# Kernel optimization log

Measured on AMD Instinct MI355X. Metric: run time of the kernel, lower is better.

## Reference

```python
import jax, jax.numpy as jnp
import numpy as np

B, D, E, H, L = 32768, 512, 10, 128, 2  # batch, input_dim, max_charts, expert hidden, latent_dim
RH1, RH2 = 256, 128                      # router hidden sizes
TAU = 3.0


def setup_inputs() -> dict:
    key = jax.random.key(0)
    ks = jax.random.split(key, 16)
    rnd = lambda k, *s: (jax.random.normal(k, s, jnp.float32) * 0.05)
    return {
        "x": jax.random.normal(ks[0], (B, D), jnp.float32),
        "u": jax.random.uniform(ks[1], (B, E), jnp.float32),
        # router params (last layer init ~ N(0, 0.01), bias 0, as in _init_router)
        "rw1": rnd(ks[2], D, RH1), "rb1": jnp.zeros((RH1,), jnp.float32),
        "rw2": rnd(ks[3], RH1, RH2), "rb2": jnp.zeros((RH2,), jnp.float32),
        "rw3": jax.random.normal(ks[4], (RH2, E), jnp.float32) * 0.01,
        "rb3": jnp.zeros((E,), jnp.float32),
        # stacked expert params: all 10 experts batched along leading dim
        "ew1": rnd(ks[5], E, D, H), "eb1": rnd(ks[6], E, H),
        "ew2": rnd(ks[7], E, H, H), "eb2": rnd(ks[8], E, H),
        "ew3": rnd(ks[9], E, H, L), "eb3": rnd(ks[10], E, L),
    }


def reference(x, u, rw1, rb1, rw2, rb2, rw3, rb3, ew1, eb1, ew2, eb2, ew3, eb3):
    # router MLP: D -> 256 -> 128 -> E
    h = jax.nn.relu(x @ rw1 + rb1)
    h = jax.nn.relu(h @ rw2 + rb2)
    logits = h @ rw3 + rb3                                  # [B, E]
    # gumbel_softmax(tau=3.0, hard=False): softmax((logits + gumbel)/tau)
    g = -jnp.log(-jnp.log(jnp.clip(u, 1e-10, 1.0)) + 1e-10)
    weights = jax.nn.softmax((logits + g) / TAU, axis=1)    # [B, E]
    # all 10 experts as batched GEMMs (fuses the python loop over charts)
    h1 = jax.nn.relu(jnp.einsum('bi,eio->beo', x, ew1) + eb1[None])   # [B, E, H]
    h2 = jax.nn.relu(jnp.einsum('beh,eho->beo', h1, ew2) + eb2[None]) # [B, E, H]
    zc = jnp.einsum('beh,ehl->bel', h2, ew3) + eb3[None]              # [B, E, L]
    z = jnp.einsum('be,bel->bl', weights, zc)                         # [B, L]
    chart_outputs = jnp.transpose(zc, (1, 0, 2))                      # [E, B, L]
    return z, weights, chart_outputs
```

## Files before the change

kernel.cpp:

```cpp
#include <hip/hip_runtime.h>
#include <stdint.h>

typedef __bf16 bf16x8 __attribute__((ext_vector_type(8)));
typedef float floatx4 __attribute__((ext_vector_type(4)));
typedef unsigned short ushort_t;

__device__ __forceinline__ ushort_t bf16rne(float f) {
    union { float f; unsigned u; } v; v.f = f;
    return (ushort_t)((v.u + 0x7fffu + ((v.u >> 16) & 1u)) >> 16);
}

__device__ __forceinline__ void gl_lds16(const ushort_t* g, ushort_t* l) {
    __builtin_amdgcn_global_load_lds(
        (const __attribute__((address_space(1))) unsigned int*)g,
        (__attribute__((address_space(3))) unsigned int*)l, 16, 0, 0);
}


#define WAIT_VM_LG_BAR(n) do { asm volatile("s_waitcnt vmcnt(" #n ") lgkmcnt(0)" ::: "memory"); __builtin_amdgcn_s_barrier(); } while (0)
#define WAIT_LG_BAR()     do { asm volatile("s_waitcnt lgkmcnt(0)" ::: "memory"); __builtin_amdgcn_s_barrier(); } while (0)

__global__ void prep(const float* __restrict__ x, ushort_t* __restrict__ x16,
                     const float* __restrict__ ew1, ushort_t* __restrict__ ew1t,
                     const float* __restrict__ ew2, ushort_t* __restrict__ ew2t,
                     const float* __restrict__ rw1, ushort_t* __restrict__ rw1t,
                     const float* __restrict__ rw2, ushort_t* __restrict__ rw2t) {
    __shared__ ushort_t sT[64 * 65];
    int b = blockIdx.x, tid = threadIdx.x;
    if (b < 16384) {
        int i = b * 256 + tid;
        float4 f = ((const float4*)x)[i];
        union { ushort_t s[4]; uint2 v; } pk;
        pk.s[0] = bf16rne(f.x); pk.s[1] = bf16rne(f.y);
        pk.s[2] = bf16rne(f.z); pk.s[3] = bf16rne(f.w);
        ((uint2*)x16)[i] = pk.v;
        return;
    }
    const float* in; ushort_t* outp; int K, N, k0, n0;
    int i = b - 16384;
    if (i < 160) {
        int e = i >> 4, t = i & 15;
        in = ew1 + e * 65536; outp = ew1t + e * 65536;
        K = 512; N = 128; k0 = (t >> 1) * 64; n0 = (t & 1) * 64;
    } else if (i < 200) {
        i -= 160; int e = i >> 2, t = i & 3;
        in = ew2 + e * 16384; outp = ew2t + e * 16384;
        K = 128; N = 128; k0 = (t >> 1) * 64; n0 = (t & 1) * 64;
    } else if (i < 232) {
        i -= 200; in = rw1; outp = rw1t;
        K = 512; N = 256; k0 = (i >> 2) * 64; n0 = (i & 3) * 64;
    } else {
        i -= 232; in = rw2; outp = rw2t;
        K = 256; N = 128; k0 = (i >> 1) * 64; n0 = (i & 1) * 64;
    }
    {
        int c = tid & 63, r0 = tid >> 6;
#pragma unroll
        for (int p = 0; p < 16; ++p) {
            int r = r0 * 16 + p;
            sT[c * 65 + r] = bf16rne(in[(size_t)(k0 + r) * N + n0 + c]);
        }
        __syncthreads();
        int rr = tid & 63, c0 = tid >> 6;
#pragma unroll
        for (int p = 0; p < 16; ++p) {
            int cc = c0 * 16 + p;
            outp[(size_t)(n0 + cc) * K + k0 + rr] = sT[cc * 65 + rr];
        }
    }
}

__global__ __launch_bounds__(256, 2)
void fused_main(const ushort_t* __restrict__ x16,
                const ushort_t* __restrict__ rw1t, const float* __restrict__ rb1,
                const ushort_t* __restrict__ rw2t, const float* __restrict__ rb2,
                const float* __restrict__ rw3, const float* __restrict__ rb3,
                const float* __restrict__ u,
                const ushort_t* __restrict__ ew1t, const ushort_t* __restrict__ ew2t,
                const float* __restrict__ eb1, const float* __restrict__ eb2,
                const float* __restrict__ ew3, const float* __restrict__ eb3,
                float* __restrict__ wts, float* __restrict__ chart) {
    __shared__ alignas(16) ushort_t sU[24576];
    __shared__ float sB1[2][128];
    __shared__ float sB2[2][128];
    __shared__ float sW3e[2][256];
    __shared__ float zbuf[128][2];

    const int tid = threadIdx.x;
    const int id = blockIdx.x;
    const int wave = tid >> 6, lane = tid & 63;
    const int ln15 = lane & 15, q = lane >> 4;
    const int wm = (wave & 1) * 64, wn = (wave >> 1) * 64;
    const int mhalf = wm >> 6, nhalf = wn >> 6;
    const int rl = lane >> 2, cl = lane & 3;
    const int sw = (cl ^ ((rl >> 1) & 3)) * 8;
    const int rg0 = wave * 2, rg1 = rg0 + 1;
    const int fslot = (4 * ln15 + (q ^ ((ln15 >> 1) & 3))) * 8;

    if (id < 256) {
        const int rb = (id & 7) * 32 + (id >> 3);
        if (tid < 128) sB2[0][tid] = rb2[tid];
        else sB2[1][tid - 128] = rb2[tid];
        const ushort_t* xblk = x16 + (size_t)rb * 128 * 512;

        auto stage_rt = [&](int dst, int k0, const ushort_t* w1base) {
            gl_lds16(xblk + (size_t)(rg0 * 16 + rl) * 512 + k0 + sw, &sU[dst + rg0 * 512]);
            gl_lds16(xblk + (size_t)(rg1 * 16 + rl) * 512 + k0 + sw, &sU[dst + rg1 * 512]);
            gl_lds16(w1base + (size_t)(rg0 * 16 + rl) * 512 + k0 + sw, &sU[dst + 4096 + rg0 * 512]);
            gl_lds16(w1base + (size_t)(rg1 * 16 + rl) * 512 + k0 + sw, &sU[dst + 4096 + rg1 * 512]);
        };
        auto stage_rw2 = [&](int dst, int kh, int ph) {
#pragma unroll
            for (int r = 0; r < 2; ++r) {
                int s = wave * 2 + r;
                gl_lds16(rw2t + (size_t)(s * 16 + rl) * 256 + ph * 128 + kh * 32 + sw,
                         &sU[dst + s * 512]);
            }
        };

        floatx4 acc2[4][4];
#pragma unroll
        for (int i = 0; i < 4; ++i)
#pragma unroll
            for (int j = 0; j < 4; ++j) acc2[i][j] = (floatx4){0.f, 0.f, 0.f, 0.f};

        auto comp_rg2 = [&](int rbase, int kh) {
            bf16x8 a[4], b[4];
#pragma unroll
            for (int t = 0; t < 4; ++t) a[t] = *(const bf16x8*)(&sU[rbase + (mhalf * 4 + t) * 512 + fslot]);
#pragma unroll
            for (int t = 0; t < 4; ++t) b[t] = *(const bf16x8*)(&sU[8192 + kh * 4096 + (nhalf * 4 + t) * 512 + lane * 8]);
            __builtin_amdgcn_s_setprio(1);
#pragma unroll
            for (int i = 0; i < 4; ++i)
#pragma unroll
                for (int j = 0; j < 4; ++j)
                    acc2[i][j] = __builtin_amdgcn_mfma_f32_16x16x32_bf16(a[i], b[j], acc2[i][j], 0, 0, 0);
            __builtin_amdgcn_s_setprio(0);
        };

        for (int ph = 0; ph < 2; ++ph) {
            const ushort_t* w1base = rw1t + (size_t)ph * 65536;
            if (tid < 128) sB1[0][tid] = rb1[ph * 128 + tid];

            floatx4 acc[4][4];
#pragma unroll
            for (int i = 0; i < 4; ++i)
#pragma unroll
                for (int j = 0; j < 4; ++j) acc[i][j] = (floatx4){0.f, 0.f, 0.f, 0.f};

            auto comp_rt = [&](int base) {
                bf16x8 a[4], b[4];
#pragma unroll
                for (int t = 0; t < 4; ++t) a[t] = *(const bf16x8*)(&sU[base + 4096 + (mhalf * 4 + t) * 512 + fslot]);
#pragma unroll
                for (int t = 0; t < 4; ++t) b[t] = *(const bf16x8*)(&sU[base + (nhalf * 4 + t) * 512 + fslot]);
                __builtin_amdgcn_s_setprio(1);
#pragma unroll
                for (int i = 0; i < 4; ++i)
#pragma unroll
                    for (int j = 0; j < 4; ++j)
                        acc[i][j] = __builtin_amdgcn_mfma_f32_16x16x32_bf16(a[i], b[j], acc[i][j], 0, 0, 0);
                __builtin_amdgcn_s_setprio(0);
            };

            stage_rt(0, 0, w1base);
            WAIT_VM_LG_BAR(0);
#pragma unroll 1
            for (int p = 0; p < 8; ++p) {
                int k0 = p * 64;
                stage_rt(8192, k0 + 32, w1base);
                comp_rt(0);
                WAIT_VM_LG_BAR(0);
                if (p < 7) {
                    stage_rt(0, k0 + 64, w1base);
                    comp_rt(8192);
                    WAIT_VM_LG_BAR(0);
                }
            }
            stage_rw2(0, 0, ph);
            comp_rt(8192);
            WAIT_LG_BAR();

#pragma unroll
            for (int i = 0; i < 4; ++i) {
                int hbase = wm + 16 * i;
                int kh = hbase >> 5;
                int qhi = (hbase >> 4) & 1;
                int slotq = 2 * qhi + (q >> 1);
                int h0 = hbase + q * 4;
#pragma unroll
                for (int j = 0; j < 4; ++j) {
                    union { ushort_t s[4]; uint2 v; } pk;
#pragma unroll
                    for (int r = 0; r < 4; ++r)
                        pk.s[r] = bf16rne(fmaxf(acc[i][j][r] + sB1[0][h0 + r], 0.f));
                    *(uint2*)(&sU[8192 + kh * 4096 + (nhalf * 4 + j) * 512 + slotq * 128 + ln15 * 8 + (q & 1) * 4]) = pk.v;
                }
            }

            WAIT_VM_LG_BAR(0);
            stage_rw2(4096, 1, ph); comp_rg2(0, 0);    WAIT_VM_LG_BAR(0);
            stage_rw2(0, 2, ph);    comp_rg2(4096, 1); WAIT_VM_LG_BAR(0);
            stage_rw2(4096, 3, ph); comp_rg2(0, 2);    WAIT_VM_LG_BAR(0);
            comp_rg2(4096, 3);
            WAIT_LG_BAR();
        }

        float* sw3r = (float*)sU;
        float* lgbuf = (float*)(&sU[2560]);
        for (int i = tid; i < 1280; i += 256) sw3r[i] = rw3[i];
        __syncthreads();

        float lg[4][10];
#pragma unroll
        for (int j = 0; j < 4; ++j)
#pragma unroll
            for (int ee = 0; ee < 10; ++ee) lg[j][ee] = 0.f;
#pragma unroll
        for (int i = 0; i < 4; ++i) {
#pragma unroll
            for (int r = 0; r < 4; ++r) {
                int n = wm + i * 16 + q * 4 + r;
                float bias = n < 128 ? sB2[0][n] : sB2[1][n - 128];
                const float* w3r = &sw3r[n * 10];
#pragma unroll
                for (int j = 0; j < 4; ++j) {
                    float val = fmaxf(acc2[i][j][r] + bias, 0.f);
#pragma unroll
                    for (int ee = 0; ee < 10; ++ee) lg[j][ee] += val * w3r[ee];
                }
            }
        }
#pragma unroll
        for (int j = 0; j < 4; ++j)
#pragma unroll
            for (int ee = 0; ee < 10; ++ee) {
                lg[j][ee] += __shfl_xor(lg[j][ee], 16, 64);
                lg[j][ee] += __shfl_xor(lg[j][ee], 32, 64);
            }
        if (wm == 0 && q == 0) {
#pragma unroll
            for (int j = 0; j < 4; ++j) {
                int row = wn + 16 * j + ln15;
#pragma unroll
                for (int ee = 0; ee < 10; ++ee) lgbuf[row * 10 + ee] = lg[j][ee];
            }
        }
        __syncthreads();
        if (wm == 64 && q == 0) {
#pragma unroll
            for (int j = 0; j < 4; ++j) {
                int row = wn + 16 * j + ln15;
#pragma unroll
                for (int ee = 0; ee < 10; ++ee) lgbuf[row * 10 + ee] += lg[j][ee];
            }
        }
        __syncthreads();
        if (tid < 128) {
            int grow = rb * 128 + tid;
            float v[10], mx = -1e30f;
#pragma unroll
            for (int ee = 0; ee < 10; ++ee) {
                float uu = u[(size_t)grow * 10 + ee];
                uu = fminf(fmaxf(uu, 1e-10f), 1.0f);
                float g = -logf(-logf(uu) + 1e-10f);
                v[ee] = (lgbuf[tid * 10 + ee] + rb3[ee] + g) * (1.0f / 3.0f);
                mx = fmaxf(mx, v[ee]);
            }
            float s = 0.f;
#pragma unroll
            for (int ee = 0; ee < 10; ++ee) { v[ee] = expf(v[ee] - mx); s += v[ee]; }
            float inv = 1.0f / s;
#pragma unroll
            for (int ee = 0; ee < 10; ++ee) wts[(size_t)grow * 10 + ee] = v[ee] * inv;
        }
    } else {
        const int eid = id - 256;
        const int xcd = eid & 7, local = eid >> 3;
        const int pr = local % 5;
        const int rb = xcd * 32 + local / 5;
        const int e0 = pr * 2;

        if (tid < 128) {
            sB1[0][tid] = eb1[e0 * 128 + tid];
            sB2[0][tid] = eb2[e0 * 128 + tid];
        } else {
            sB1[1][tid - 128] = eb1[(e0 + 1) * 128 + (tid - 128)];
            sB2[1][tid - 128] = eb2[(e0 + 1) * 128 + (tid - 128)];
        }
        sW3e[0][tid] = ew3[e0 * 256 + tid];
        sW3e[1][tid] = ew3[(e0 + 1) * 256 + tid];

        const ushort_t* xblk = x16 + (size_t)rb * 128 * 512;
        const ushort_t* w1a = ew1t + (size_t)e0 * 65536;
        const ushort_t* w1b = w1a + 65536;

        floatx4 accA[4][4], accB[4][4];
#pragma unroll
        for (int i = 0; i < 4; ++i)
#pragma unroll
            for (int j = 0; j < 4; ++j) {
                accA[i][j] = (floatx4){0.f, 0.f, 0.f, 0.f};
                accB[i][j] = (floatx4){0.f, 0.f, 0.f, 0.f};
            }

        auto stage_g1 = [&](int dst, int k0) {
            gl_lds16(xblk + (size_t)(rg0 * 16 + rl) * 512 + k0 + sw, &sU[dst + rg0 * 512]);
            gl_lds16(xblk + (size_t)(rg1 * 16 + rl) * 512 + k0 + sw, &sU[dst + rg1 * 512]);
            gl_lds16(w1a + (size_t)(rg0 * 16 + rl) * 512 + k0 + sw, &sU[dst + 4096 + rg0 * 512]);
            gl_lds16(w1a + (size_t)(rg1 * 16 + rl) * 512 + k0 + sw, &sU[dst + 4096 + rg1 * 512]);
            gl_lds16(w1b + (size_t)(rg0 * 16 + rl) * 512 + k0 + sw, &sU[dst + 8192 + rg0 * 512]);
            gl_lds16(w1b + (size_t)(rg1 * 16 + rl) * 512 + k0 + sw, &sU[dst + 8192 + rg1 * 512]);
        };
        auto comp_g1 = [&](int base) {
            bf16x8 a0[4], a1[4], b[4];
#pragma unroll
            for (int t = 0; t < 4; ++t) b[t] = *(const bf16x8*)(&sU[base + (nhalf * 4 + t) * 512 + fslot]);
#pragma unroll
            for (int t = 0; t < 4; ++t) a0[t] = *(const bf16x8*)(&sU[base + 4096 + (mhalf * 4 + t) * 512 + fslot]);
#pragma unroll
            for (int t = 0; t < 4; ++t) a1[t] = *(const bf16x8*)(&sU[base + 8192 + (mhalf * 4 + t) * 512 + fslot]);
            __builtin_amdgcn_s_setprio(1);
#pragma unroll
            for (int i = 0; i < 4; ++i)
#pragma unroll
                for (int j = 0; j < 4; ++j) {
                    accA[i][j] = __builtin_amdgcn_mfma_f32_16x16x32_bf16(a0[i], b[j], accA[i][j], 0, 0, 0);
                    accB[i][j] = __builtin_amdgcn_mfma_f32_16x16x32_bf16(a1[i], b[j], accB[i][j], 0, 0, 0);
                }
            __builtin_amdgcn_s_setprio(0);
        };
        auto stage_w2 = [&](const ushort_t* w2, int dst, int kh) {
#pragma unroll
            for (int r = 0; r < 2; ++r) {
                int s = wave * 2 + r;
                gl_lds16(w2 + (size_t)(s * 16 + rl) * 128 + kh * 32 + sw, &sU[dst + s * 512]);
            }
        };
        auto comp_g2 = [&](int rbase, int kh, floatx4 (&acc2)[4][4]) {
            bf16x8 a[4], b[4];
#pragma unroll
            for (int t = 0; t < 4; ++t) a[t] = *(const bf16x8*)(&sU[rbase + (mhalf * 4 + t) * 512 + fslot]);
#pragma unroll
            for (int t = 0; t < 4; ++t) b[t] = *(const bf16x8*)(&sU[8192 + kh * 4096 + (nhalf * 4 + t) * 512 + lane * 8]);
            __builtin_amdgcn_s_setprio(1);
#pragma unroll
            for (int i = 0; i < 4; ++i)
#pragma unroll
                for (int j = 0; j < 4; ++j)
                    acc2[i][j] = __builtin_amdgcn_mfma_f32_16x16x32_bf16(a[i], b[j], acc2[i][j], 0, 0, 0);
            __builtin_amdgcn_s_setprio(0);
        };

        stage_g1(0, 0);
        WAIT_VM_LG_BAR(0);
#pragma unroll 1
        for (int p = 0; p < 8; ++p) {
            int k0 = p * 64;
            stage_g1(12288, k0 + 32);
            comp_g1(0);
            WAIT_VM_LG_BAR(0);
            if (p < 7) {
                stage_g1(0, k0 + 64);
                comp_g1(12288);
                WAIT_VM_LG_BAR(0);
            }
        }
        stage_w2(ew2t + (size_t)e0 * 16384, 0, 0);
        comp_g1(12288);
        WAIT_LG_BAR();

#pragma unroll
        for (int ex = 0; ex < 2; ++ex) {
            const int e = e0 + ex;
            const ushort_t* w2 = ew2t + (size_t)e * 16384;

#pragma unroll
            for (int i = 0; i < 4; ++i) {
                int hbase = wm + 16 * i;
                int kh = hbase >> 5;
                int qhi = (hbase >> 4) & 1;
                int slotq = 2 * qhi + (q >> 1);
                int h0 = hbase + q * 4;
#pragma unroll
                for (int j = 0; j < 4; ++j) {
                    union { ushort_t s[4]; uint2 v; } pk;
#pragma unroll
                    for (int r = 0; r < 4; ++r) {
                        float av = ex == 0 ? accA[i][j][r] : accB[i][j][r];
                        pk.s[r] = bf16rne(fmaxf(av + sB1[ex][h0 + r], 0.f));
                    }
                    *(uint2*)(&sU[8192 + kh * 4096 + (nhalf * 4 + j) * 512 + slotq * 128 + ln15 * 8 + (q & 1) * 4]) = pk.v;
                }
            }

            floatx4 acc2[4][4];
#pragma unroll
            for (int i = 0; i < 4; ++i)
#pragma unroll
                for (int j = 0; j < 4; ++j) acc2[i][j] = (floatx4){0.f, 0.f, 0.f, 0.f};

            WAIT_VM_LG_BAR(0);
            stage_w2(w2, 4096, 1); comp_g2(0, 0, acc2);    WAIT_VM_LG_BAR(0);
            stage_w2(w2, 0, 2);    comp_g2(4096, 1, acc2); WAIT_VM_LG_BAR(0);
            stage_w2(w2, 4096, 3); comp_g2(0, 2, acc2);    WAIT_VM_LG_BAR(0);
            if (ex == 0) stage_w2(ew2t + (size_t)(e0 + 1) * 16384, 0, 0);
            comp_g2(4096, 3, acc2);

            float zc0[4] = {0.f, 0.f, 0.f, 0.f}, zc1[4] = {0.f, 0.f, 0.f, 0.f};
#pragma unroll
            for (int i = 0; i < 4; ++i) {
                int o0 = wm + i * 16 + q * 4;
#pragma unroll
                for (int r = 0; r < 4; ++r) {
                    int o = o0 + r;
                    float w3a = sW3e[ex][2 * o], w3b = sW3e[ex][2 * o + 1];
                    float bias = sB2[ex][o];
#pragma unroll
                    for (int j = 0; j < 4; ++j) {
                        float val = fmaxf(acc2[i][j][r] + bias, 0.f);
                        zc0[j] += val * w3a;
                        zc1[j] += val * w3b;
                    }
                }
            }
#pragma unroll
            for (int j = 0; j < 4; ++j) {
                zc0[j] += __shfl_xor(zc0[j], 16, 64);
                zc0[j] += __shfl_xor(zc0[j], 32, 64);
                zc1[j] += __shfl_xor(zc1[j], 16, 64);
                zc1[j] += __shfl_xor(zc1[j], 32, 64);
            }
            if (wm == 0 && q == 0) {
#pragma unroll
                for (int j = 0; j < 4; ++j) {
                    int row = wn + j * 16 + ln15;
                    zbuf[row][0] = zc0[j];
                    zbuf[row][1] = zc1[j];
                }
            }
            __syncthreads();
            if (wm == 64 && q == 0) {
#pragma unroll
                for (int j = 0; j < 4; ++j) {
                    int row = wn + j * 16 + ln15;
                    zbuf[row][0] += zc0[j];
                    zbuf[row][1] += zc1[j];
                }
            }
            __syncthreads();
            {
                int row = tid >> 1, l = tid & 1;
                int grow = rb * 128 + row;
                chart[(size_t)e * 65536 + (size_t)grow * 2 + l] = zbuf[row][l] + eb3[e * 2 + l];
            }
        }
    }
}

__global__ void z_final(const float* __restrict__ w, const float* __restrict__ chart,
                        float* __restrict__ z) {
    __shared__ float swt[2560];
    int b0 = blockIdx.x * 256;
    for (int i = threadIdx.x; i < 2560; i += 256) swt[i] = w[(size_t)b0 * 10 + i];
    __syncthreads();
    int row = b0 + threadIdx.x;
    float z0 = 0.f, z1 = 0.f;
#pragma unroll
    for (int e = 0; e < 10; ++e) {
        float we = swt[threadIdx.x * 10 + e];
        float2 c = *(const float2*)(&chart[(size_t)e * 65536 + (size_t)row * 2]);
        z0 += we * c.x;
        z1 += we * c.y;
    }
    float2 o; o.x = z0; o.y = z1;
    *(float2*)(&z[(size_t)row * 2]) = o;
}

extern "C" void kernel_launch(void* const* d_in, const int* in_sizes, int n_in,
                              void* d_out, int out_size, void* d_ws, size_t ws_size,
                              hipStream_t stream) {
    const float* x = (const float*)d_in[0];
    const float* u = (const float*)d_in[1];
    const float* rw1 = (const float*)d_in[2];
    const float* rb1 = (const float*)d_in[3];
    const float* rw2 = (const float*)d_in[4];
    const float* rb2 = (const float*)d_in[5];
    const float* rw3 = (const float*)d_in[6];
    const float* rb3 = (const float*)d_in[7];
    const float* ew1 = (const float*)d_in[8];
    const float* eb1 = (const float*)d_in[9];
    const float* ew2 = (const float*)d_in[10];
    const float* eb2 = (const float*)d_in[11];
    const float* ew3 = (const float*)d_in[12];
    const float* eb3 = (const float*)d_in[13];
    float* out = (float*)d_out;
    float* z = out;
    float* wts = out + 65536;
    float* chart = out + 393216;

    ushort_t* x16  = (ushort_t*)d_ws;
    ushort_t* ew1t = x16 + 16777216;
    ushort_t* ew2t = ew1t + 655360;
    ushort_t* rw1t = ew2t + 163840;
    ushort_t* rw2t = rw1t + 131072;

    prep<<<16624, 256, 0, stream>>>(x, x16, ew1, ew1t, ew2, ew2t, rw1, rw1t, rw2, rw2t);

    fused_main<<<1536, 256, 0, stream>>>(x16, rw1t, rb1, rw2t, rb2, rw3, rb3, u,
                                         ew1t, ew2t, eb1, eb2, ew3, eb3,
                                         wts, chart);

    z_final<<<128, 256, 0, stream>>>(wts, chart, z);
}
```

Baseline: 205.8 us.

## Triple-buffer K-loop staging and halve second-layer stage/barrier count

Grows the shared buffer so the first-layer GEMM loops in both router and expert paths use three LDS stages with partial vmcnt waits, keeping two loads in flight instead of one. The second-layer weight staging now loads two K-chunks per stage, so four stage/barrier rounds become two. Router bias loading is hoisted out of the phase loop. Larger LDS use (about 72KB per block) may limit occupancy at two blocks per CU.

```diff
diff --git a/kernel.cpp b/kernel.cpp
--- a/kernel.cpp
+++ b/kernel.cpp
@@ -80,7 +80,7 @@
                 const float* __restrict__ eb1, const float* __restrict__ eb2,
                 const float* __restrict__ ew3, const float* __restrict__ eb3,
                 float* __restrict__ wts, float* __restrict__ chart) {
-    __shared__ alignas(16) ushort_t sU[24576];
+    __shared__ alignas(16) ushort_t sU[36864];
     __shared__ float sB1[2][128];
     __shared__ float sB2[2][128];
     __shared__ float sW3e[2][256];
@@ -99,6 +99,7 @@
 
     if (id < 256) {
         const int rb = (id & 7) * 32 + (id >> 3);
+        sB1[tid >> 7][tid & 127] = rb1[tid];
         if (tid < 128) sB2[0][tid] = rb2[tid];
         else sB2[1][tid - 128] = rb2[tid];
         const ushort_t* xblk = x16 + (size_t)rb * 128 * 512;
@@ -109,12 +110,14 @@
             gl_lds16(w1base + (size_t)(rg0 * 16 + rl) * 512 + k0 + sw, &sU[dst + 4096 + rg0 * 512]);
             gl_lds16(w1base + (size_t)(rg1 * 16 + rl) * 512 + k0 + sw, &sU[dst + 4096 + rg1 * 512]);
         };
-        auto stage_rw2 = [&](int dst, int kh, int ph) {
-#pragma unroll
-            for (int r = 0; r < 2; ++r) {
-                int s = wave * 2 + r;
-                gl_lds16(rw2t + (size_t)(s * 16 + rl) * 256 + ph * 128 + kh * 32 + sw,
-                         &sU[dst + s * 512]);
+        auto stage_rw2 = [&](int reg, int half, int ph) {
+#pragma unroll
+            for (int r = 0; r < 4; ++r) {
+                int s = wave * 4 + r;
+                int khl = s >> 3, rg = s & 7;
+                int kh = half * 2 + khl;
+                gl_lds16(rw2t + (size_t)(rg * 16 + rl) * 256 + ph * 128 + kh * 32 + sw,
+                         &sU[reg + s * 512]);
             }
         };
 
@@ -124,24 +127,27 @@
 #pragma unroll
             for (int j = 0; j < 4; ++j) acc2[i][j] = (floatx4){0.f, 0.f, 0.f, 0.f};
 
-        auto comp_rg2 = [&](int rbase, int kh) {
-            bf16x8 a[4], b[4];
-#pragma unroll
-            for (int t = 0; t < 4; ++t) a[t] = *(const bf16x8*)(&sU[rbase + (mhalf * 4 + t) * 512 + fslot]);
-#pragma unroll
-            for (int t = 0; t < 4; ++t) b[t] = *(const bf16x8*)(&sU[8192 + kh * 4096 + (nhalf * 4 + t) * 512 + lane * 8]);
-            __builtin_amdgcn_s_setprio(1);
-#pragma unroll
-            for (int i = 0; i < 4; ++i)
-#pragma unroll
-                for (int j = 0; j < 4; ++j)
-                    acc2[i][j] = __builtin_amdgcn_mfma_f32_16x16x32_bf16(a[i], b[j], acc2[i][j], 0, 0, 0);
-            __builtin_amdgcn_s_setprio(0);
+        auto comp_rg2 = [&](int reg, int half) {
+#pragma unroll
+            for (int khl = 0; khl < 2; ++khl) {
+                int kh = half * 2 + khl;
+                bf16x8 a[4], b[4];
+#pragma unroll
+                for (int t = 0; t < 4; ++t) a[t] = *(const bf16x8*)(&sU[reg + (khl * 8 + mhalf * 4 + t) * 512 + fslot]);
+#pragma unroll
+                for (int t = 0; t < 4; ++t) b[t] = *(const bf16x8*)(&sU[8192 + kh * 4096 + (nhalf * 4 + t) * 512 + lane * 8]);
+                __builtin_amdgcn_s_setprio(1);
+#pragma unroll
+                for (int i = 0; i < 4; ++i)
+#pragma unroll
+                    for (int j = 0; j < 4; ++j)
+                        acc2[i][j] = __builtin_amdgcn_mfma_f32_16x16x32_bf16(a[i], b[j], acc2[i][j], 0, 0, 0);
+                __builtin_amdgcn_s_setprio(0);
+            }
         };
 
         for (int ph = 0; ph < 2; ++ph) {
             const ushort_t* w1base = rw1t + (size_t)ph * 65536;
-            if (tid < 128) sB1[0][tid] = rb1[ph * 128 + tid];
 
             floatx4 acc[4][4];
 #pragma unroll
@@ -165,22 +171,19 @@
             };
 
             stage_rt(0, 0, w1base);
-            WAIT_VM_LG_BAR(0);
+            stage_rt(8192, 32, w1base);
+            int cb = 0, sb = 16384;
 #pragma unroll 1
-            for (int p = 0; p < 8; ++p) {
-                int k0 = p * 64;
-                stage_rt(8192, k0 + 32, w1base);
-                comp_rt(0);
-                WAIT_VM_LG_BAR(0);
-                if (p < 7) {
-                    stage_rt(0, k0 + 64, w1base);
-                    comp_rt(8192);
-                    WAIT_VM_LG_BAR(0);
-                }
-            }
+            for (int p = 0; p < 16; ++p) {
+                if (p < 15) { WAIT_VM_LG_BAR(4); } else { WAIT_VM_LG_BAR(0); }
+                if (p < 14) stage_rt(sb, (p + 2) * 32, w1base);
+                comp_rt(cb);
+                cb = cb == 16384 ? 0 : cb + 8192;
+                sb = sb == 16384 ? 0 : sb + 8192;
+            }
+            WAIT_LG_BAR();
+
             stage_rw2(0, 0, ph);
-            comp_rt(8192);
-            WAIT_LG_BAR();
 
 #pragma unroll
             for (int i = 0; i < 4; ++i) {
@@ -194,16 +197,16 @@
                     union { ushort_t s[4]; uint2 v; } pk;
 #pragma unroll
                     for (int r = 0; r < 4; ++r)
-                        pk.s[r] = bf16rne(fmaxf(acc[i][j][r] + sB1[0][h0 + r], 0.f));
+                        pk.s[r] = bf16rne(fmaxf(acc[i][j][r] + sB1[ph][h0 + r], 0.f));
                     *(uint2*)(&sU[8192 + kh * 4096 + (nhalf * 4 + j) * 512 + slotq * 128 + ln15 * 8 + (q & 1) * 4]) = pk.v;
                 }
             }
 
             WAIT_VM_LG_BAR(0);
-            stage_rw2(4096, 1, ph); comp_rg2(0, 0);    WAIT_VM_LG_BAR(0);
-            stage_rw2(0, 2, ph);    comp_rg2(4096, 1); WAIT_VM_LG_BAR(0);
-            stage_rw2(4096, 3, ph); comp_rg2(0, 2);    WAIT_VM_LG_BAR(0);
-            comp_rg2(4096, 3);
+            stage_rw2(24576, 1, ph);
+            comp_rg2(0, 0);
+            WAIT_VM_LG_BAR(0);
+            comp_rg2(24576, 1);
             WAIT_LG_BAR();
         }
 
@@ -331,45 +334,48 @@
                 }
             __builtin_amdgcn_s_setprio(0);
         };
-        auto stage_w2 = [&](const ushort_t* w2, int dst, int kh) {
-#pragma unroll
-            for (int r = 0; r < 2; ++r) {
-                int s = wave * 2 + r;
-                gl_lds16(w2 + (size_t)(s * 16 + rl) * 128 + kh * 32 + sw, &sU[dst + s * 512]);
-            }
-        };
-        auto comp_g2 = [&](int rbase, int kh, floatx4 (&acc2)[4][4]) {
-            bf16x8 a[4], b[4];
-#pragma unroll
-            for (int t = 0; t < 4; ++t) a[t] = *(const bf16x8*)(&sU[rbase + (mhalf * 4 + t) * 512 + fslot]);
-#pragma unroll
-            for (int t = 0; t < 4; ++t) b[t] = *(const bf16x8*)(&sU[8192 + kh * 4096 + (nhalf * 4 + t) * 512 + lane * 8]);
-            __builtin_amdgcn_s_setprio(1);
-#pragma unroll
-            for (int i = 0; i < 4; ++i)
-#pragma unroll
-                for (int j = 0; j < 4; ++j)
-                    acc2[i][j] = __builtin_amdgcn_mfma_f32_16x16x32_bf16(a[i], b[j], acc2[i][j], 0, 0, 0);
-            __builtin_amdgcn_s_setprio(0);
+        auto stage_w2 = [&](const ushort_t* w2, int reg, int half) {
+#pragma unroll
+            for (int r = 0; r < 4; ++r) {
+                int s = wave * 4 + r;
+                int khl = s >> 3, rg = s & 7;
+                int kh = half * 2 + khl;
+                gl_lds16(w2 + (size_t)(rg * 16 + rl) * 128 + kh * 32 + sw, &sU[reg + s * 512]);
+            }
+        };
+        auto comp_g2 = [&](int reg, int half, floatx4 (&acc2)[4][4]) {
+#pragma unroll
+            for (int khl = 0; khl < 2; ++khl) {
+                int kh = half * 2 + khl;
+                bf16x8 a[4], b[4];
+#pragma unroll
+                for (int t = 0; t < 4; ++t) a[t] = *(const bf16x8*)(&sU[reg + (khl * 8 + mhalf * 4 + t) * 512 + fslot]);
+#pragma unroll
+                for (int t = 0; t < 4; ++t) b[t] = *(const bf16x8*)(&sU[8192 + kh * 4096 + (nhalf * 4 + t) * 512 + lane * 8]);
+                __builtin_amdgcn_s_setprio(1);
+#pragma unroll
+                for (int i = 0; i < 4; ++i)
+#pragma unroll
+                    for (int j = 0; j < 4; ++j)
+                        acc2[i][j] = __builtin_amdgcn_mfma_f32_16x16x32_bf16(a[i], b[j], acc2[i][j], 0, 0, 0);
+                __builtin_amdgcn_s_setprio(0);
+            }
         };
 
         stage_g1(0, 0);
-        WAIT_VM_LG_BAR(0);
+        stage_g1(12288, 32);
+        int cb = 0, sb = 24576;
 #pragma unroll 1
-        for (int p = 0; p < 8; ++p) {
-            int k0 = p * 64;
-            stage_g1(12288, k0 + 32);
-            comp_g1(0);
-            WAIT_VM_LG_BAR(0);
-            if (p < 7) {
-                stage_g1(0, k0 + 64);
-                comp_g1(12288);
-                WAIT_VM_LG_BAR(0);
-            }
-        }
+        for (int p = 0; p < 16; ++p) {
+            if (p < 15) { WAIT_VM_LG_BAR(6); } else { WAIT_VM_LG_BAR(0); }
+            if (p < 14) stage_g1(sb, (p + 2) * 32);
+            comp_g1(cb);
+            cb = cb == 24576 ? 0 : cb + 12288;
+            sb = sb == 24576 ? 0 : sb + 12288;
+        }
+        WAIT_LG_BAR();
+
         stage_w2(ew2t + (size_t)e0 * 16384, 0, 0);
-        comp_g1(12288);
-        WAIT_LG_BAR();
 
 #pragma unroll
         for (int ex = 0; ex < 2; ++ex) {
@@ -402,11 +408,11 @@
                 for (int j = 0; j < 4; ++j) acc2[i][j] = (floatx4){0.f, 0.f, 0.f, 0.f};
 
             WAIT_VM_LG_BAR(0);
-            stage_w2(w2, 4096, 1); comp_g2(0, 0, acc2);    WAIT_VM_LG_BAR(0);
-            stage_w2(w2, 0, 2);    comp_g2(4096, 1, acc2); WAIT_VM_LG_BAR(0);
-            stage_w2(w2, 4096, 3); comp_g2(0, 2, acc2);    WAIT_VM_LG_BAR(0);
+            stage_w2(w2, 24576, 1);
+            comp_g2(0, 0, acc2);
+            WAIT_VM_LG_BAR(0);
             if (ex == 0) stage_w2(ew2t + (size_t)(e0 + 1) * 16384, 0, 0);
-            comp_g2(4096, 3, acc2);
+            comp_g2(24576, 1, acc2);
 
             float zc0[4] = {0.f, 0.f, 0.f, 0.f}, zc1[4] = {0.f, 0.f, 0.f, 0.f};
 #pragma unroll
```

New measurement: 207.4 us. No clear change (+0.8%).

## Overlap expert-0 layer-3 reduction with expert-1 GEMM2 and use packed bf16 convert

Applied to the files above, without the earlier changes.

Unrolls the two-expert loop so expert 0's third-layer dot products, the cross-wave zbuf reduction and the chart store are interleaved with expert 1's second GEMM stages. This removes two dedicated __syncthreads per block by reusing the pipeline barriers. It also replaces the manual round-to-nearest bf16 conversion with the hardware v_cvt_pk_bf16_f32 instruction. Keeping a second 4x4 accumulator set live raises register pressure, which could lower occupancy or cause spills.

```diff
diff --git a/kernel.cpp b/kernel.cpp
--- a/kernel.cpp
+++ b/kernel.cpp
@@ -8,6 +8,12 @@
 __device__ __forceinline__ ushort_t bf16rne(float f) {
     union { float f; unsigned u; } v; v.f = f;
     return (ushort_t)((v.u + 0x7fffu + ((v.u >> 16) & 1u)) >> 16);
+}
+
+__device__ __forceinline__ unsigned cvt_pk_bf16(float lo, float hi) {
+    unsigned r;
+    asm("v_cvt_pk_bf16_f32 %0, %1, %2" : "=v"(r) : "v"(lo), "v"(hi));
+    return r;
 }
 
 __device__ __forceinline__ void gl_lds16(const ushort_t* g, ushort_t* l) {
@@ -191,11 +197,14 @@
                 int h0 = hbase + q * 4;
 #pragma unroll
                 for (int j = 0; j < 4; ++j) {
-                    union { ushort_t s[4]; uint2 v; } pk;
-#pragma unroll
-                    for (int r = 0; r < 4; ++r)
-                        pk.s[r] = bf16rne(fmaxf(acc[i][j][r] + sB1[0][h0 + r], 0.f));
-                    *(uint2*)(&sU[8192 + kh * 4096 + (nhalf * 4 + j) * 512 + slotq * 128 + ln15 * 8 + (q & 1) * 4]) = pk.v;
+                    float v0 = fmaxf(acc[i][j][0] + sB1[0][h0 + 0], 0.f);
+                    float v1 = fmaxf(acc[i][j][1] + sB1[0][h0 + 1], 0.f);
+                    float v2 = fmaxf(acc[i][j][2] + sB1[0][h0 + 2], 0.f);
+                    float v3 = fmaxf(acc[i][j][3] + sB1[0][h0 + 3], 0.f);
+                    uint2 pk;
+                    pk.x = cvt_pk_bf16(v0, v1);
+                    pk.y = cvt_pk_bf16(v2, v3);
+                    *(uint2*)(&sU[8192 + kh * 4096 + (nhalf * 4 + j) * 512 + slotq * 128 + ln15 * 8 + (q & 1) * 4]) = pk;
                 }
             }
 
@@ -337,20 +346,6 @@
                 int s = wave * 2 + r;
                 gl_lds16(w2 + (size_t)(s * 16 + rl) * 128 + kh * 32 + sw, &sU[dst + s * 512]);
             }
-        };
-        auto comp_g2 = [&](int rbase, int kh, floatx4 (&acc2)[4][4]) {
-            bf16x8 a[4], b[4];
-#pragma unroll
-            for (int t = 0; t < 4; ++t) a[t] = *(const bf16x8*)(&sU[rbase + (mhalf * 4 + t) * 512 + fslot]);
-#pragma unroll
-            for (int t = 0; t < 4; ++t) b[t] = *(const bf16x8*)(&sU[8192 + kh * 4096 + (nhalf * 4 + t) * 512 + lane * 8]);
-            __builtin_amdgcn_s_setprio(1);
-#pragma unroll
-            for (int i = 0; i < 4; ++i)
-#pragma unroll
-                for (int j = 0; j < 4; ++j)
-                    acc2[i][j] = __builtin_amdgcn_mfma_f32_16x16x32_bf16(a[i], b[j], acc2[i][j], 0, 0, 0);
-            __builtin_amdgcn_s_setprio(0);
         };
 
         stage_g1(0, 0);
@@ -371,11 +366,24 @@
         comp_g1(12288);
         WAIT_LG_BAR();
 
-#pragma unroll
-        for (int ex = 0; ex < 2; ++ex) {
-            const int e = e0 + ex;
-            const ushort_t* w2 = ew2t + (size_t)e * 16384;
-
+        const ushort_t* w2_0 = ew2t + (size_t)e0 * 16384;
+        const ushort_t* w2_1 = w2_0 + 16384;
+
+        auto comp_g2 = [&](int rbase, int kh, floatx4 (&acc2)[4][4]) {
+            bf16x8 a[4], b[4];
+#pragma unroll
+            for (int t = 0; t < 4; ++t) a[t] = *(const bf16x8*)(&sU[rbase + (mhalf * 4 + t) * 512 + fslot]);
+#pragma unroll
+            for (int t = 0; t < 4; ++t) b[t] = *(const bf16x8*)(&sU[8192 + kh * 4096 + (nhalf * 4 + t) * 512 + lane * 8]);
+            __builtin_amdgcn_s_setprio(1);
+#pragma unroll
+            for (int i = 0; i < 4; ++i)
+#pragma unroll
+                for (int j = 0; j < 4; ++j)
+                    acc2[i][j] = __builtin_amdgcn_mfma_f32_16x16x32_bf16(a[i], b[j], acc2[i][j], 0, 0, 0);
+            __builtin_amdgcn_s_setprio(0);
+        };
+        auto epilogue = [&](floatx4 (&acc)[4][4], int ex) {
 #pragma unroll
             for (int i = 0; i < 4; ++i) {
                 int hbase = wm + 16 * i;
@@ -385,30 +393,20 @@
                 int h0 = hbase + q * 4;
 #pragma unroll
                 for (int j = 0; j < 4; ++j) {
-                    union { ushort_t s[4]; uint2 v; } pk;
-#pragma unroll
-                    for (int r = 0; r < 4; ++r) {
-                        float av = ex == 0 ? accA[i][j][r] : accB[i][j][r];
-                        pk.s[r] = bf16rne(fmaxf(av + sB1[ex][h0 + r], 0.f));
-                    }
-                    *(uint2*)(&sU[8192 + kh * 4096 + (nhalf * 4 + j) * 512 + slotq * 128 + ln15 * 8 + (q & 1) * 4]) = pk.v;
+                    float v0 = fmaxf(acc[i][j][0] + sB1[ex][h0 + 0], 0.f);
+                    float v1 = fmaxf(acc[i][j][1] + sB1[ex][h0 + 1], 0.f);
+                    float v2 = fmaxf(acc[i][j][2] + sB1[ex][h0 + 2], 0.f);
+                    float v3 = fmaxf(acc[i][j][3] + sB1[ex][h0 + 3], 0.f);
+                    uint2 pk;
+                    pk.x = cvt_pk_bf16(v0, v1);
+                    pk.y = cvt_pk_bf16(v2, v3);
+                    *(uint2*)(&sU[8192 + kh * 4096 + (nhalf * 4 + j) * 512 + slotq * 128 + ln15 * 8 + (q & 1) * 4]) = pk;
                 }
             }
-
-            floatx4 acc2[4][4];
-#pragma unroll
-            for (int i = 0; i < 4; ++i)
-#pragma unroll
-                for (int j = 0; j < 4; ++j) acc2[i][j] = (floatx4){0.f, 0.f, 0.f, 0.f};
-
-            WAIT_VM_LG_BAR(0);
-            stage_w2(w2, 4096, 1); comp_g2(0, 0, acc2);    WAIT_VM_LG_BAR(0);
-            stage_w2(w2, 0, 2);    comp_g2(4096, 1, acc2); WAIT_VM_LG_BAR(0);
-            stage_w2(w2, 4096, 3); comp_g2(0, 2, acc2);    WAIT_VM_LG_BAR(0);
-            if (ex == 0) stage_w2(ew2t + (size_t)(e0 + 1) * 16384, 0, 0);
-            comp_g2(4096, 3, acc2);
-
-            float zc0[4] = {0.f, 0.f, 0.f, 0.f}, zc1[4] = {0.f, 0.f, 0.f, 0.f};
+        };
+        auto gemm3 = [&](floatx4 (&acc2)[4][4], int ex, float (&zc0)[4], float (&zc1)[4]) {
+#pragma unroll
+            for (int j = 0; j < 4; ++j) { zc0[j] = 0.f; zc1[j] = 0.f; }
 #pragma unroll
             for (int i = 0; i < 4; ++i) {
                 int o0 = wm + i * 16 + q * 4;
@@ -432,30 +430,83 @@
                 zc1[j] += __shfl_xor(zc1[j], 16, 64);
                 zc1[j] += __shfl_xor(zc1[j], 32, 64);
             }
-            if (wm == 0 && q == 0) {
-#pragma unroll
-                for (int j = 0; j < 4; ++j) {
-                    int row = wn + j * 16 + ln15;
-                    zbuf[row][0] = zc0[j];
-                    zbuf[row][1] = zc1[j];
-                }
-            }
-            __syncthreads();
-            if (wm == 64 && q == 0) {
-#pragma unroll
-                for (int j = 0; j < 4; ++j) {
-                    int row = wn + j * 16 + ln15;
-                    zbuf[row][0] += zc0[j];
-                    zbuf[row][1] += zc1[j];
-                }
-            }
-            __syncthreads();
-            {
-                int row = tid >> 1, l = tid & 1;
-                int grow = rb * 128 + row;
-                chart[(size_t)e * 65536 + (size_t)grow * 2 + l] = zbuf[row][l] + eb3[e * 2 + l];
-            }
-        }
+        };
+        auto chart_write = [&](int e) {
+            int row = tid >> 1, l = tid & 1;
+            int grow = rb * 128 + row;
+            chart[(size_t)e * 65536 + (size_t)grow * 2 + l] = zbuf[row][l] + eb3[e * 2 + l];
+        };
+
+        floatx4 acc20[4][4], acc21[4][4];
+#pragma unroll
+        for (int i = 0; i < 4; ++i)
+#pragma unroll
+            for (int j = 0; j < 4; ++j) {
+                acc20[i][j] = (floatx4){0.f, 0.f, 0.f, 0.f};
+                acc21[i][j] = (floatx4){0.f, 0.f, 0.f, 0.f};
+            }
+
+        epilogue(accA, 0);
+        WAIT_VM_LG_BAR(0);
+        stage_w2(w2_0, 4096, 1); comp_g2(0, 0, acc20);    WAIT_VM_LG_BAR(0);
+        stage_w2(w2_0, 0, 2);    comp_g2(4096, 1, acc20); WAIT_VM_LG_BAR(0);
+        stage_w2(w2_0, 4096, 3); comp_g2(0, 2, acc20);    WAIT_VM_LG_BAR(0);
+        stage_w2(w2_1, 0, 0);    comp_g2(4096, 3, acc20);
+        WAIT_LG_BAR();
+
+        epilogue(accB, 1);
+        WAIT_VM_LG_BAR(0);
+
+        float zc0[4], zc1[4];
+        stage_w2(w2_1, 4096, 1);
+        comp_g2(0, 0, acc21);
+        gemm3(acc20, 0, zc0, zc1);
+        if (wm == 0 && q == 0) {
+#pragma unroll
+            for (int j = 0; j < 4; ++j) {
+                int row = wn + j * 16 + ln15;
+                zbuf[row][0] = zc0[j];
+                zbuf[row][1] = zc1[j];
+            }
+        }
+        WAIT_VM_LG_BAR(0);
+        stage_w2(w2_1, 0, 2);
+        comp_g2(4096, 1, acc21);
+        if (wm == 64 && q == 0) {
+#pragma unroll
+            for (int j = 0; j < 4; ++j) {
+                int row = wn + j * 16 + ln15;
+                zbuf[row][0] += zc0[j];
+                zbuf[row][1] += zc1[j];
+            }
+        }
+        WAIT_VM_LG_BAR(0);
+        stage_w2(w2_1, 4096, 3);
+        comp_g2(0, 2, acc21);
+        chart_write(e0);
+        WAIT_VM_LG_BAR(0);
+        comp_g2(4096, 3, acc21);
+
+        gemm3(acc21, 1, zc0, zc1);
+        if (wm == 0 && q == 0) {
+#pragma unroll
+            for (int j = 0; j < 4; ++j) {
+                int row = wn + j * 16 + ln15;
+                zbuf[row][0] = zc0[j];
+                zbuf[row][1] = zc1[j];
+            }
+        }
+        __syncthreads();
+        if (wm == 64 && q == 0) {
+#pragma unroll
+            for (int j = 0; j < 4; ++j) {
+                int row = wn + j * 16 + ln15;
+                zbuf[row][0] += zc0[j];
+                zbuf[row][1] += zc1[j];
+            }
+        }
+        __syncthreads();
+        chart_write(e0 + 1);
     }
 }
 
```

Measured after the change: 207.2 us. No clear change (+0.7%).
